# Kernel optimization log

Measured on AMD Instinct MI355X. Metric: run time of the kernel, lower is better.

The kernel has to match this reference:

```python
import jax, jax.numpy as jnp
import numpy as np
from jax import lax

B, S, W, T = 64, 256, 32, 32
DEFAULT_TAG = 0
NEG = -1e30


def _input_likelihood(logits, text_mask, transitions, start_tr, end_tr):
    # logits: (B, S, W, T); forward algorithm over all segmentations (log-semiring DP)
    Bb, Ss, Ww, Tt = logits.shape
    logits_t = jnp.transpose(logits, (1, 2, 0, 3))  # (S, W, B, T)
    lengths = text_mask.sum(axis=1)  # (B,)
    d_idx = jnp.arange(Ww)

    def step(buf, inp):
        # buf[k] = alpha[j - k]; buf[0] = alpha[j]
        j, emit = inp  # emit: (W, B, T)
        # span of width d+1 ending at j, preceded by a segment ending at j-d-1
        trans_part = jax.nn.logsumexp(buf[:, :, :, None] + transitions[None, None], axis=2) + emit
        start_part = emit + start_tr  # span covering 0..j (d == j)
        inner = jnp.where((d_idx == j)[:, None, None], start_part, trans_part)
        inner = jnp.where((d_idx <= j)[:, None, None], inner, NEG)
        alpha_nxt = jax.nn.logsumexp(inner, axis=0)  # (B, T)
        alpha_nxt = jnp.where((j < lengths)[:, None], alpha_nxt, buf[0])
        buf = jnp.concatenate([alpha_nxt[None], buf[:-1]], axis=0)
        return buf, None

    buf0 = jnp.zeros((Ww, Bb, Tt), logits.dtype)
    buf, _ = lax.scan(step, buf0, (jnp.arange(Ss), logits_t))
    return jax.nn.logsumexp(buf[0] + end_tr, axis=-1)  # (B,)


def _joint_likelihood(logits, tags, text_mask, transitions, start_tr, end_tr):
    Bb, Ss, Ww, Tt = logits.shape
    j = jnp.arange(Ss)[:, None]
    d = jnp.arange(Ww)[None, :]
    valid_jd = (d <= j).astype(logits.dtype)  # original skips d > j
    tm = text_mask.astype(logits.dtype)  # (B, S)
    valid_tag = (tags != DEFAULT_TAG).astype(logits.dtype)  # (B, S, W)
    emit = jnp.take_along_axis(logits, tags[..., None], axis=-1)[..., 0]
    emit = emit * valid_tag * tm[:, :, None]
    start_score = start_tr[tags]  # (B, S, W), used where d == j
    prev_j = jnp.clip(j - d - 1, 0, Ss - 1)  # (S, W)
    prev_tags = tags[:, prev_j, :]  # (B, S, W, W)
    trans = transitions[prev_tags, tags[..., None]]  # (B, S, W, W)
    prev_valid = (prev_tags != DEFAULT_TAG).astype(logits.dtype)
    trans_sum = jnp.sum(prev_valid * trans, axis=-1)  # (B, S, W)
    trans_score = jnp.where(d == j, start_score, jnp.where(d < j, trans_sum, 0.0))
    score = (trans_score * tm[:, :, None] + emit) * valid_jd
    numerator = jnp.sum(score, axis=(1, 2))  # (B,)
    last_idx = text_mask.sum(axis=1) - 1  # (B,)
    last_tags = tags[jnp.arange(Bb), last_idx]  # (B, W)
    last_valid = (last_tags != DEFAULT_TAG).astype(logits.dtype)
    numerator = numerator + jnp.sum(last_valid * end_tr[last_tags], axis=1)
    return numerator


def setup_inputs() -> dict:
    key = jax.random.key(0)
    k1, k2, k3, k4, k5 = jax.random.split(key, 5)
    inputs = jax.random.normal(k1, (B, S, W, T), jnp.float32)
    tags = jax.random.randint(k2, (B, S, W), 0, T, dtype=jnp.int32)
    mask = jnp.ones((B, S), jnp.int32)
    xavier_std = (2.0 / (T + T)) ** 0.5
    transitions = jax.random.normal(k3, (T, T), jnp.float32) * xavier_std
    start_transitions = jax.random.normal(k4, (T,), jnp.float32)
    end_transitions = jax.random.normal(k5, (T,), jnp.float32)
    return dict(inputs=inputs, tags=tags, mask=mask, transitions=transitions,
                start_transitions=start_transitions, end_transitions=end_transitions)


def reference(inputs, tags, mask, transitions, start_transitions, end_transitions):
    log_num = _joint_likelihood(inputs, tags, mask, transitions, start_transitions, end_transitions)
    log_den = _input_likelihood(inputs, mask, transitions, start_transitions, end_transitions)
    log_loss = log_num - log_den  # (B,)
    batch_loss = jnp.sum(log_loss) / inputs.shape[0]
    return batch_loss, log_num
```

## Files before the change

### kernel.cpp

```cpp
#include <hip/hip_runtime.h>

#define S_ 256
#define W_ 32
#define T_ 32
#define B_ 64

#define SCAN_STEP(J, U, SP)                                                    \
  {                                                                            \
    const int sl_ = ((U) + 1) & 3;                                             \
    const int eb_ = (U) & 1;                                                   \
    _Pragma("unroll")                                                          \
    for (int i_ = 0; i_ < 16; ++i_) Ee[eb_ ^ 1][i_] = __expf(raw[sl_][i_]);    \
    {                                                                          \
      int pl_ = (J) + 5; pl_ = (pl_ > 255) ? 255 : pl_;                        \
      const float* src_ = lpB + (size_t)pl_ * 1024;                            \
      _Pragma("unroll")                                                        \
      for (int i_ = 0; i_ < 16; ++i_) raw[sl_][i_] = src_[i_ * 32];            \
    }                                                                          \
    float a0_ = M[1] * Ee[eb_][1], a1_ = M[2] * Ee[eb_][2];                    \
    float a2_ = M[3] * Ee[eb_][3], a3_ = M[4] * Ee[eb_][4];                    \
    a0_ = fmaf(M[5],  Ee[eb_][5],  a0_); a1_ = fmaf(M[6],  Ee[eb_][6],  a1_);  \
    a2_ = fmaf(M[7],  Ee[eb_][7],  a2_); a3_ = fmaf(M[8],  Ee[eb_][8],  a3_);  \
    a0_ = fmaf(M[9],  Ee[eb_][9],  a0_); a1_ = fmaf(M[10], Ee[eb_][10], a1_);  \
    a2_ = fmaf(M[11], Ee[eb_][11], a2_); a3_ = fmaf(M[12], Ee[eb_][12], a3_);  \
    a0_ = fmaf(M[13], Ee[eb_][13], a0_); a1_ = fmaf(M[14], Ee[eb_][14], a1_);  \
    a2_ = fmaf(M[15], Ee[eb_][15], a2_);                                       \
    float db_   = (a0_ + a1_) + (a2_ + a3_);                                   \
    float part_ = fmaf(y, Ee[eb_][0], db_);                                    \
    float full_ = part_ + __shfl_xor(part_, 32, 64);                           \
    if (SP) {                                                                  \
      full_ += __expf(stt + eS[(U)] - m_ref);                                  \
      if ((J) + 4 < 32) eS[(U)] = lp[((J) + 4) * 1056 + t];                    \
    }                                                                          \
    g2[eb_][t] = full_;                                                        \
    float s0_  = __uint_as_float(                                              \
        __builtin_amdgcn_readfirstlane(__float_as_uint(full_)));               \
    float rcp_ = __builtin_amdgcn_rcpf(s0_);                                   \
    m_ref += __logf(s0_);                                                      \
    float4 v0_ = *(const float4*)&g2[eb_][16 * h + 0];                         \
    float4 v1_ = *(const float4*)&g2[eb_][16 * h + 4];                         \
    float4 v2_ = *(const float4*)&g2[eb_][16 * h + 8];                         \
    float4 v3_ = *(const float4*)&g2[eb_][16 * h + 12];                        \
    float qa_ = v0_.x * Ec[0], qb_ = v0_.y * Ec[1];                            \
    float qc_ = v0_.z * Ec[2], qd_ = v0_.w * Ec[3];                            \
    qa_ = fmaf(v1_.x, Ec[4],  qa_); qb_ = fmaf(v1_.y, Ec[5],  qb_);            \
    qc_ = fmaf(v1_.z, Ec[6],  qc_); qd_ = fmaf(v1_.w, Ec[7],  qd_);            \
    qa_ = fmaf(v2_.x, Ec[8],  qa_); qb_ = fmaf(v2_.y, Ec[9],  qb_);            \
    qc_ = fmaf(v2_.z, Ec[10], qc_); qd_ = fmaf(v2_.w, Ec[11], qd_);            \
    qa_ = fmaf(v3_.x, Ec[12], qa_); qb_ = fmaf(v3_.y, Ec[13], qb_);            \
    qc_ = fmaf(v3_.z, Ec[14], qc_); qd_ = fmaf(v3_.w, Ec[15], qd_);            \
    float qo_ = (qa_ + qb_) + (qc_ + qd_);                                     \
    float qs_ = qo_ + __shfl_xor(qo_, 32, 64);                                 \
    float t15_ = M[15] * rcp_;                                                 \
    float sw_  = __shfl_xor(t15_, 32, 64);                                     \
    _Pragma("unroll")                                                          \
    for (int i_ = 15; i_ >= 2; --i_) M[i_] = M[i_ - 1] * rcp_;                 \
    M[1] = y * rcp_;                                                           \
    y = h ? sw_ : qs_ * rcp_;                                                  \
  }

__global__ __launch_bounds__(512, 2) void smcrf_fused(
    const float* __restrict__ logits,
    const int*   __restrict__ tags,
    const float* __restrict__ transitions,
    const float* __restrict__ start_tr,
    const float* __restrict__ end_tr,
    float*       __restrict__ out,
    float*       __restrict__ log_den)
{
  const int bx  = blockIdx.x;
  const int tid = threadIdx.x;

  __shared__ int   s_tags[S_ * W_];
  __shared__ float s_rs[S_ * T_];
  __shared__ float s_trans[T_ * T_];
  __shared__ float s_start[T_];
  __shared__ float s_end[T_];
  __shared__ float s_part[8];
  __shared__ __align__(16) float g2[2][32];

  if (bx >= B_) {
    const int b    = bx - B_;
    const int lane = tid & 63;
    const int wave = tid >> 6;
    const int t    = tid & 31;

    for (int i = tid; i < S_ * W_; i += 512) s_tags[i] = tags[b * (S_ * W_) + i];
    for (int i = tid; i < T_ * T_; i += 512) s_trans[i] = transitions[i];
    if (tid < T_) { s_start[tid] = start_tr[tid]; s_end[tid] = end_tr[tid]; }
    __syncthreads();

    const size_t lbase = (size_t)b * (S_ * (size_t)(W_ * T_));

    for (int pj = (tid >> 5); pj < S_; pj += 16) {
      int tagv = s_tags[pj * W_ + t];
      float sum = 0.f;
      #pragma unroll
      for (int w = 0; w < W_; ++w) {
        int pt = __shfl(tagv, w, 32);
        float v = s_trans[pt * T_ + t];
        sum += (pt != 0) ? v : 0.f;
      }
      s_rs[pj * T_ + t] = sum;
    }
    __syncthreads();

    float acc = 0.f;
    for (int pr = tid; pr < S_ * W_; pr += 512) {
      int j = pr >> 5, d = pr & 31;
      if (d > j) continue;
      int tg2 = s_tags[pr];
      float e = logits[lbase + (size_t)pr * T_ + tg2];
      e = (tg2 != 0) ? e : 0.f;
      float ts = (d == j) ? s_start[tg2] : s_rs[(j - d - 1) * T_ + tg2];
      acc += ts + e;
    }
    if (tid < 32) {
      int lt = s_tags[255 * W_ + tid];
      acc += (lt != 0) ? s_end[lt] : 0.f;
    }
    #pragma unroll
    for (int off = 32; off > 0; off >>= 1) acc += __shfl_down(acc, off, 64);
    if (lane == 0) s_part[wave] = acc;
    __syncthreads();
    if (tid == 0) {
      float tot = 0.f;
      #pragma unroll
      for (int wv = 0; wv < 8; ++wv) tot += s_part[wv];
      out[1 + b] = tot;
    }
    return;
  }

  if (tid >= 64) return;
  const int b    = bx;
  const int lane = tid;
  const int t    = lane & 31;
  const int h    = lane >> 5;

  const float* lp  = logits + (size_t)b * (S_ * (size_t)(W_ * T_));
  const float* lpB = lp + (16 * h) * 32 + t;

  float Ec[16];
  #pragma unroll
  for (int i = 0; i < 16; ++i) Ec[i] = __expf(transitions[(16 * h + i) * 32 + t]);
  const float stt = start_tr[t];
  const float ett = end_tr[t];

  float M[16];
  #pragma unroll
  for (int i = 0; i < 16; ++i) M[i] = 0.f;
  float y = 0.f;
  float m_ref = 0.f;

  float raw[4][16];
  #pragma unroll
  for (int p = 0; p < 4; ++p) {
    const float* src = lpB + p * 1024;
    #pragma unroll
    for (int i = 0; i < 16; ++i) raw[p][i] = src[i * 32];
  }
  float eS[4];
  #pragma unroll
  for (int p = 0; p < 4; ++p) eS[p] = lp[p * 1056 + t];

  float Ee[2][16];
  #pragma unroll
  for (int i = 0; i < 16; ++i) Ee[0][i] = __expf(raw[0][i]);
  {
    const float* src = lpB + 4 * 1024;
    #pragma unroll
    for (int i = 0; i < 16; ++i) raw[0][i] = src[i * 32];
  }

  for (int j0 = 0; j0 < 32; j0 += 4) {
    SCAN_STEP(j0 + 0, 0, true)
    SCAN_STEP(j0 + 1, 1, true)
    SCAN_STEP(j0 + 2, 2, true)
    SCAN_STEP(j0 + 3, 3, true)
  }
  for (int j0 = 32; j0 < 252; j0 += 4) {
    SCAN_STEP(j0 + 0, 0, false)
    SCAN_STEP(j0 + 1, 1, false)
    SCAN_STEP(j0 + 2, 2, false)
    SCAN_STEP(j0 + 3, 3, false)
  }
  SCAN_STEP(252, 0, false)
  SCAN_STEP(253, 1, false)
  SCAN_STEP(254, 2, false)

  {
    float a0_ = M[1] * Ee[1][1], a1_ = M[2] * Ee[1][2];
    float a2_ = M[3] * Ee[1][3], a3_ = M[4] * Ee[1][4];
    a0_ = fmaf(M[5],  Ee[1][5],  a0_); a1_ = fmaf(M[6],  Ee[1][6],  a1_);
    a2_ = fmaf(M[7],  Ee[1][7],  a2_); a3_ = fmaf(M[8],  Ee[1][8],  a3_);
    a0_ = fmaf(M[9],  Ee[1][9],  a0_); a1_ = fmaf(M[10], Ee[1][10], a1_);
    a2_ = fmaf(M[11], Ee[1][11], a2_); a3_ = fmaf(M[12], Ee[1][12], a3_);
    a0_ = fmaf(M[13], Ee[1][13], a0_); a1_ = fmaf(M[14], Ee[1][14], a1_);
    a2_ = fmaf(M[15], Ee[1][15], a2_);
    float db_   = (a0_ + a1_) + (a2_ + a3_);
    float part_ = fmaf(y, Ee[1][0], db_);
    float full_ = part_ + __shfl_xor(part_, 32, 64);
    float alpha = m_ref + __logf(full_);

    float z  = alpha + ett;
    float zm = z;
    zm = fmaxf(zm, __shfl_xor(zm, 1, 64));
    zm = fmaxf(zm, __shfl_xor(zm, 2, 64));
    zm = fmaxf(zm, __shfl_xor(zm, 4, 64));
    zm = fmaxf(zm, __shfl_xor(zm, 8, 64));
    zm = fmaxf(zm, __shfl_xor(zm, 16, 64));
    float zs = __expf(z - zm);
    zs += __shfl_xor(zs, 1, 64);
    zs += __shfl_xor(zs, 2, 64);
    zs += __shfl_xor(zs, 4, 64);
    zs += __shfl_xor(zs, 8, 64);
    zs += __shfl_xor(zs, 16, 64);
    if (lane == 0) log_den[b] = zm + __logf(zs);
  }
}

__global__ void smcrf_loss(const float* __restrict__ log_den,
                           float* __restrict__ out)
{
  int tv = threadIdx.x;
  float v = out[1 + tv] - log_den[tv];
  #pragma unroll
  for (int off = 32; off > 0; off >>= 1) v += __shfl_down(v, off, 64);
  if (tv == 0) out[0] = v * (1.0f / 64.0f);
}

extern "C" void kernel_launch(void* const* d_in, const int* in_sizes, int n_in,
                              void* d_out, int out_size, void* d_ws, size_t ws_size,
                              hipStream_t stream) {
  const float* logits      = (const float*)d_in[0];
  const int*   tags        = (const int*)d_in[1];
  const float* transitions = (const float*)d_in[3];
  const float* start_trans = (const float*)d_in[4];
  const float* end_trans   = (const float*)d_in[5];
  float* out     = (float*)d_out;
  float* log_den = (float*)d_ws;

  hipLaunchKernelGGL(smcrf_fused, dim3(2 * B_), dim3(512), 0, stream,
                     logits, tags, transitions, start_trans, end_trans, out, log_den);
  hipLaunchKernelGGL(smcrf_loss, dim3(1), dim3(64), 0, stream, log_den, out);
}
```

Before: 182.3 us.

## Offload emission exp to producer waves via LDS ring with flag sync

The scan block now uses four extra producer waves that load logits, compute the exponentials and write them into an 8-slot shared-memory ring. Handoff to the single consumer wave, which runs the serial DP, goes through volatile ready flags and a progress counter. The start-transition term is rebuilt from the already-exponentiated plane using a running rescale factor instead of a separate exp per step. This takes the exp and global-load latency off the serial critical path, at the cost of busy-wait spinning, more LDS use and reliance on ordering through volatile shared accesses without fences.

```diff
diff --git a/kernel.cpp b/kernel.cpp
--- a/kernel.cpp
+++ b/kernel.cpp
@@ -5,42 +5,47 @@
 #define T_ 32
 #define B_ 64
 
-#define SCAN_STEP(J, U, SP)                                                    \
+#define CSTEP(J, P, SP)                                                        \
   {                                                                            \
-    const int sl_ = ((U) + 1) & 3;                                             \
-    const int eb_ = (U) & 1;                                                   \
-    _Pragma("unroll")                                                          \
-    for (int i_ = 0; i_ < 16; ++i_) Ee[eb_ ^ 1][i_] = __expf(raw[sl_][i_]);    \
-    {                                                                          \
-      int pl_ = (J) + 5; pl_ = (pl_ > 255) ? 255 : pl_;                        \
-      const float* src_ = lpB + (size_t)pl_ * 1024;                            \
+    if ((J) < 255) {                                                           \
+      if (!ok_next) {                                                          \
+        volatile int* f_ = &p_flag[((J) + 1) & 7];                             \
+        while (*f_ != (J) + 1) {}                                              \
+      }                                                                        \
+    }                                                                          \
+    int fl2_ = ((J) < 254) ? *(volatile int*)&p_flag[((J) + 2) & 7] : 0;       \
+    if ((J) < 255) {                                                           \
+      const float* src_ = &eplane[(((J) + 1) & 7) * 1056 + t * 33 + 16 * h];   \
       _Pragma("unroll")                                                        \
-      for (int i_ = 0; i_ < 16; ++i_) raw[sl_][i_] = src_[i_ * 32];            \
-    }                                                                          \
-    float a0_ = M[1] * Ee[eb_][1], a1_ = M[2] * Ee[eb_][2];                    \
-    float a2_ = M[3] * Ee[eb_][3], a3_ = M[4] * Ee[eb_][4];                    \
-    a0_ = fmaf(M[5],  Ee[eb_][5],  a0_); a1_ = fmaf(M[6],  Ee[eb_][6],  a1_);  \
-    a2_ = fmaf(M[7],  Ee[eb_][7],  a2_); a3_ = fmaf(M[8],  Ee[eb_][8],  a3_);  \
-    a0_ = fmaf(M[9],  Ee[eb_][9],  a0_); a1_ = fmaf(M[10], Ee[eb_][10], a1_);  \
-    a2_ = fmaf(M[11], Ee[eb_][11], a2_); a3_ = fmaf(M[12], Ee[eb_][12], a3_);  \
-    a0_ = fmaf(M[13], Ee[eb_][13], a0_); a1_ = fmaf(M[14], Ee[eb_][14], a1_);  \
-    a2_ = fmaf(M[15], Ee[eb_][15], a2_);                                       \
+      for (int i_ = 0; i_ < 16; ++i_) Ee[(P) ^ 1][i_] = src_[i_];              \
+    }                                                                          \
+    float a0_ = M[1] * Ee[P][1], a1_ = M[2] * Ee[P][2];                        \
+    float a2_ = M[3] * Ee[P][3], a3_ = M[4] * Ee[P][4];                        \
+    a0_ = fmaf(M[5],  Ee[P][5],  a0_); a1_ = fmaf(M[6],  Ee[P][6],  a1_);      \
+    a2_ = fmaf(M[7],  Ee[P][7],  a2_); a3_ = fmaf(M[8],  Ee[P][8],  a3_);      \
+    a0_ = fmaf(M[9],  Ee[P][9],  a0_); a1_ = fmaf(M[10], Ee[P][10], a1_);      \
+    a2_ = fmaf(M[11], Ee[P][11], a2_); a3_ = fmaf(M[12], Ee[P][12], a3_);      \
+    a0_ = fmaf(M[13], Ee[P][13], a0_); a1_ = fmaf(M[14], Ee[P][14], a1_);      \
+    a2_ = fmaf(M[15], Ee[P][15], a2_);                                         \
     float db_   = (a0_ + a1_) + (a2_ + a3_);                                   \
-    float part_ = fmaf(y, Ee[eb_][0], db_);                                    \
+    float part_ = fmaf(y, Ee[P][0], db_);                                      \
     float full_ = part_ + __shfl_xor(part_, 32, 64);                           \
     if (SP) {                                                                  \
-      full_ += __expf(stt + eS[(U)] - m_ref);                                  \
-      if ((J) + 4 < 32) eS[(U)] = lp[((J) + 4) * 1056 + t];                    \
-    }                                                                          \
-    g2[eb_][t] = full_;                                                        \
-    float s0_  = __uint_as_float(                                              \
+      float v_ = Ee[P][(J) & 15];                                              \
+      float o_ = __shfl_xor(v_, 32, 64);                                       \
+      float sel_ = ((J) < 16) ? (h ? o_ : v_) : (h ? v_ : o_);                 \
+      full_ = fmaf(estt * r_run, sel_, full_);                                 \
+    }                                                                          \
+    if (lane < 32) g2[P][t] = full_;                                           \
+    float s0_ = __uint_as_float(                                               \
         __builtin_amdgcn_readfirstlane(__float_as_uint(full_)));               \
     float rcp_ = __builtin_amdgcn_rcpf(s0_);                                   \
     m_ref += __logf(s0_);                                                      \
-    float4 v0_ = *(const float4*)&g2[eb_][16 * h + 0];                         \
-    float4 v1_ = *(const float4*)&g2[eb_][16 * h + 4];                         \
-    float4 v2_ = *(const float4*)&g2[eb_][16 * h + 8];                         \
-    float4 v3_ = *(const float4*)&g2[eb_][16 * h + 12];                        \
+    if (SP) r_run *= rcp_;                                                     \
+    float4 v0_ = *(const float4*)&g2[P][16 * h + 0];                           \
+    float4 v1_ = *(const float4*)&g2[P][16 * h + 4];                           \
+    float4 v2_ = *(const float4*)&g2[P][16 * h + 8];                           \
+    float4 v3_ = *(const float4*)&g2[P][16 * h + 12];                          \
     float qa_ = v0_.x * Ec[0], qb_ = v0_.y * Ec[1];                            \
     float qc_ = v0_.z * Ec[2], qd_ = v0_.w * Ec[3];                            \
     qa_ = fmaf(v1_.x, Ec[4],  qa_); qb_ = fmaf(v1_.y, Ec[5],  qb_);            \
@@ -57,6 +62,26 @@
     for (int i_ = 15; i_ >= 2; --i_) M[i_] = M[i_ - 1] * rcp_;                 \
     M[1] = y * rcp_;                                                           \
     y = h ? sw_ : qs_ * rcp_;                                                  \
+    ok_next = (fl2_ == (J) + 2);                                               \
+    if (lane == 0) *(volatile int*)&c_prog = (J);                              \
+  }
+
+#define PSTEP(p, BUF)                                                          \
+  {                                                                            \
+    {                                                                          \
+      volatile int* cp_ = &c_prog;                                             \
+      while (*cp_ < (p) - 8) {}                                                \
+    }                                                                          \
+    float* dst_ = &eplane[((p) & 7) * 1056];                                   \
+    _Pragma("unroll")                                                          \
+    for (int c_ = 0; c_ < 16; ++c_)                                            \
+      dst_[(lane & 31) * 33 + (lane >> 5) + 2 * c_] = __expf(BUF[c_]);         \
+    if (lane == 0) *(volatile int*)&p_flag[(p) & 7] = (p);                     \
+    if ((p) + 8 < 256) {                                                       \
+      const float* s_ = lp + ((p) + 8) * 1024 + lane;                          \
+      _Pragma("unroll")                                                        \
+      for (int c_ = 0; c_ < 16; ++c_) BUF[c_] = s_[c_ * 64];                   \
+    }                                                                          \
   }
 
 __global__ __launch_bounds__(512, 2) void smcrf_fused(
@@ -78,6 +103,9 @@
   __shared__ float s_end[T_];
   __shared__ float s_part[8];
   __shared__ __align__(16) float g2[2][32];
+  __shared__ float eplane[8 * 1056];
+  __shared__ int   p_flag[8];
+  __shared__ int   c_prog;
 
   if (bx >= B_) {
     const int b    = bx - B_;
@@ -132,62 +160,72 @@
     return;
   }
 
-  if (tid >= 64) return;
   const int b    = bx;
-  const int lane = tid;
+  const int wv   = tid >> 6;
+  const int lane = tid & 63;
   const int t    = lane & 31;
   const int h    = lane >> 5;
-
-  const float* lp  = logits + (size_t)b * (S_ * (size_t)(W_ * T_));
-  const float* lpB = lp + (16 * h) * 32 + t;
+  const float* lp = logits + (size_t)b * (S_ * (size_t)(W_ * T_));
+
+  if (tid < 8) p_flag[tid] = -1;
+  if (tid == 8) c_prog = -1;
+  __syncthreads();
+  if (wv >= 5) return;
+
+  if (wv >= 1) {
+    const int p0 = wv - 1;
+    float A[16], B[16];
+    {
+      const float* sA = lp + p0 * 1024 + lane;
+      #pragma unroll
+      for (int c = 0; c < 16; ++c) A[c] = sA[c * 64];
+      const float* sB = lp + (p0 + 4) * 1024 + lane;
+      #pragma unroll
+      for (int c = 0; c < 16; ++c) B[c] = sB[c * 64];
+    }
+    for (int p = p0; p < 256; p += 8) {
+      PSTEP(p, A)
+      PSTEP(p + 4, B)
+    }
+    return;
+  }
 
   float Ec[16];
   #pragma unroll
   for (int i = 0; i < 16; ++i) Ec[i] = __expf(transitions[(16 * h + i) * 32 + t]);
-  const float stt = start_tr[t];
-  const float ett = end_tr[t];
+  const float stt  = start_tr[t];
+  const float ett  = end_tr[t];
+  const float estt = __expf(stt);
 
   float M[16];
   #pragma unroll
   for (int i = 0; i < 16; ++i) M[i] = 0.f;
-  float y = 0.f;
-  float m_ref = 0.f;
-
-  float raw[4][16];
-  #pragma unroll
-  for (int p = 0; p < 4; ++p) {
-    const float* src = lpB + p * 1024;
+  float y = 0.f, m_ref = 0.f, r_run = 1.f;
+
+  float Ee[2][16];
+  {
+    volatile int* f0 = &p_flag[0];
+    while (*f0 != 0) {}
+    const float* src = &eplane[0 * 1056 + t * 33 + 16 * h];
     #pragma unroll
-    for (int i = 0; i < 16; ++i) raw[p][i] = src[i * 32];
-  }
-  float eS[4];
-  #pragma unroll
-  for (int p = 0; p < 4; ++p) eS[p] = lp[p * 1056 + t];
-
-  float Ee[2][16];
-  #pragma unroll
-  for (int i = 0; i < 16; ++i) Ee[0][i] = __expf(raw[0][i]);
-  {
-    const float* src = lpB + 4 * 1024;
-    #pragma unroll
-    for (int i = 0; i < 16; ++i) raw[0][i] = src[i * 32];
-  }
-
-  for (int j0 = 0; j0 < 32; j0 += 4) {
-    SCAN_STEP(j0 + 0, 0, true)
-    SCAN_STEP(j0 + 1, 1, true)
-    SCAN_STEP(j0 + 2, 2, true)
-    SCAN_STEP(j0 + 3, 3, true)
-  }
-  for (int j0 = 32; j0 < 252; j0 += 4) {
-    SCAN_STEP(j0 + 0, 0, false)
-    SCAN_STEP(j0 + 1, 1, false)
-    SCAN_STEP(j0 + 2, 2, false)
-    SCAN_STEP(j0 + 3, 3, false)
-  }
-  SCAN_STEP(252, 0, false)
-  SCAN_STEP(253, 1, false)
-  SCAN_STEP(254, 2, false)
+    for (int i = 0; i < 16; ++i) Ee[0][i] = src[i];
+  }
+  bool ok_next = (*(volatile int*)&p_flag[1] == 1);
+
+  CSTEP(0,0,1)  CSTEP(1,1,1)  CSTEP(2,0,1)  CSTEP(3,1,1)
+  CSTEP(4,0,1)  CSTEP(5,1,1)  CSTEP(6,0,1)  CSTEP(7,1,1)
+  CSTEP(8,0,1)  CSTEP(9,1,1)  CSTEP(10,0,1) CSTEP(11,1,1)
+  CSTEP(12,0,1) CSTEP(13,1,1) CSTEP(14,0,1) CSTEP(15,1,1)
+  CSTEP(16,0,1) CSTEP(17,1,1) CSTEP(18,0,1) CSTEP(19,1,1)
+  CSTEP(20,0,1) CSTEP(21,1,1) CSTEP(22,0,1) CSTEP(23,1,1)
+  CSTEP(24,0,1) CSTEP(25,1,1) CSTEP(26,0,1) CSTEP(27,1,1)
+  CSTEP(28,0,1) CSTEP(29,1,1) CSTEP(30,0,1) CSTEP(31,1,1)
+
+  for (int j0 = 32; j0 < 254; j0 += 2) {
+    CSTEP(j0, 0, 0)
+    CSTEP(j0 + 1, 1, 0)
+  }
+  CSTEP(254, 0, 0)
 
   {
     float a0_ = M[1] * Ee[1][1], a1_ = M[2] * Ee[1][2];
```

Result: no change. 185.8 us (+1.9%).
